# Performance work log

Hardware: AMD Instinct MI355X
Metric: run time of the kernel (lower is better)

## Reference

```python
import jax, jax.numpy as jnp
import numpy as np

INF = 99999.0  # sentinel used by the original torch module


def _dtw_table(x, y):
    """Full (N+1, M+1) DTW DP table, identical math to the torch double loop.

    Row recurrence: r[j+1] = c[j] + min(prev[j+1], prev[j], r[j]).
    Rewritten as the min-plus linear recurrence r[j+1] = min(a[j] + r[j], b[j])
    with a[j] = c[j], b[j] = c[j] + min(prev[j+1], prev[j]), which is
    associative and solved per-row with lax.associative_scan (wavefront-free
    parallelism within each row); rows advance with lax.scan.
    """
    M = y.shape[0]
    dt = x.dtype
    row0 = jnp.full((M + 1,), INF, dtype=dt).at[0].set(0.0)  # dtw[0, :]
    inf1 = jnp.full((1,), INF, dtype=dt)

    def combine(l, r):
        a1, b1 = l
        a2, b2 = r
        return (a1 + a2, jnp.minimum(a2 + b1, b2))

    def step(prev, xi):
        c = (xi - y) ** 2                              # (M,) squared cost
        m = jnp.minimum(prev[1:], prev[:-1])           # min(dtw[i,j+1], dtw[i,j])
        A, B = jax.lax.associative_scan(combine, (c, c + m))
        r = jnp.minimum(A + INF, B)                    # r[0] = INF folded in
        row = jnp.concatenate([inf1, r])               # dtw[i+1, :]
        return row, row

    _, rows = jax.lax.scan(step, row0, x)              # (N, M+1)
    table = jnp.concatenate([row0[None, :], rows], axis=0)
    return jnp.sqrt(table)


def setup_inputs() -> dict:
    key = jax.random.key(0)
    kx, ky = jax.random.split(key)
    N = M = 6144
    x = jax.random.normal(kx, (N,), dtype=jnp.float32)
    y = jax.random.normal(ky, (M,), dtype=jnp.float32)
    return {"x": x, "y": y}


def reference(x, y):
    return _dtw_table(x, y)
```

## Files before the change

### kernel.cpp

```cpp
#include <hip/hip_runtime.h>
#include <math.h>

#define NN    6144
#define MP1   6145
#define R     4
#define KC    4
#define WCH   (KC * 64)
#define GCH   (NN / WCH)
#define RTS   16
#define NWS   (NN / R)
#define STEPS (NWS + 63)
#define FINF  99999.0f

#define BR     384
#define NBI    (NN / BR)
#define TS2    (BR / R)
#define STEPS2 (TS2 + 63)

typedef float f4a __attribute__((ext_vector_type(4), aligned(4)));
typedef float f4v __attribute__((ext_vector_type(4), aligned(16)));

__device__ __forceinline__ float readlane_f(float v, int l) {
    return __int_as_float(__builtin_amdgcn_readlane(__float_as_int(v), l));
}
__device__ __forceinline__ float shup1(float v) {
    return __int_as_float(__builtin_amdgcn_update_dpp(
        0, __float_as_int(v), 0x138, 0xF, 0xF, false));
}

__global__ void __launch_bounds__(64) dtw_bnd(const float* __restrict__ x,
                                              const float* __restrict__ y,
                                              int* __restrict__ flags,
                                              float* __restrict__ bnd,
                                              float* __restrict__ rowb) {
    const int g    = blockIdx.x;
    const int lane = threadIdx.x;
    const int j0   = g * WCH;
    const int c0   = j0 + lane * KC;

    float yv[KC], cur[KC];
#pragma unroll
    for (int q = 0; q < KC; ++q) {
        yv[q]  = y[c0 + q];
        cur[q] = FINF;
    }
    float pl = (c0 == 0) ? 0.0f : FINF;
    float rlast[R];
#pragma unroll
    for (int r = 0; r < R; ++r) rlast[r] = FINF;
    float vbuf = FINF, vnext = FINF;

    const float4* x4 = (const float4*)x;
    float4 xw  = x4[lane];
    float4 xwN = x4[64 + lane];
    float xcur[R];
#pragma unroll
    for (int r = 0; r < R; ++r) xcur[r] = x[r];

    float cnx[R][KC];
#pragma unroll
    for (int r = 0; r < R; ++r)
#pragma unroll
        for (int q = 0; q < KC; ++q) {
            const float d = xcur[r] - yv[q];
            cnx[r][q] = d * d;
        }

    if (g != 0) {
        while (__hip_atomic_load(&flags[(g - 1) * 16], __ATOMIC_ACQUIRE,
                                 __HIP_MEMORY_SCOPE_AGENT) < 1) {
            __builtin_amdgcn_s_sleep(1);
        }
        vnext = bnd[(size_t)(g - 1) * NN + lane];
    }

    for (int s = 0; s < STEPS; ++s) {
        if (g != 0 && s < NWS && (s & (RTS - 1)) == 0) vbuf = vnext;

        if (g != 0 && (s & (RTS - 1)) == RTS - 4 && (s + 4) < NWS) {
            const int want = ((s + 4) >> 4) + 1;
            while (__hip_atomic_load(&flags[(g - 1) * 16], __ATOMIC_ACQUIRE,
                                     __HIP_MEMORY_SCOPE_AGENT) < want) {
                __builtin_amdgcn_s_sleep(1);
            }
            vnext = bnd[(size_t)(g - 1) * NN + (size_t)R * (s + 4) + lane];
        }

        float vin[R];
#pragma unroll
        for (int r = 0; r < R; ++r) {
            const float up = shup1(rlast[r]);
            const float vb = readlane_f(vbuf, ((s & (RTS - 1)) << 2) + r);
            const float l0 = (g == 0) ? FINF : vb;
            vin[r] = (lane == 0) ? l0 : up;
        }

        const bool active = (s >= lane) && (s - lane < NWS);
        if (active) {
#pragma unroll
            for (int r = 0; r < R; ++r) {
                float rl  = vin[r];
                float pm1 = (r == 0) ? pl : vin[r - 1];
                float nv[KC];
#pragma unroll
                for (int q = 0; q < KC; ++q) {
                    const float upv = cur[q];
                    rl     = cnx[r][q] + fminf(fminf(rl, upv), pm1);
                    pm1    = upv;
                    cur[q] = rl;
                    nv[q]  = rl;
                }
                rlast[r] = rl;
                if (r == R - 1) {
                    const int tp1 = s - lane + 1;
                    const int k   = tp1 / 96;
                    if (k * 96 == tp1 && k >= 1 && k <= NBI - 1) {
                        *(f4a*)&rowb[(size_t)k * MP1 + c0 + 1] =
                            (f4a){nv[0], nv[1], nv[2], nv[3]};
                    }
                }
            }
            pl = vin[R - 1];
            if (lane == 63) {
                *(f4a*)&bnd[(size_t)g * NN + R * (s - 63)] =
                    (f4a){rlast[0], rlast[1], rlast[2], rlast[3]};
            }
        }

        const int sn = s + 1;
        if ((sn & 63) == 0) {
            xw = xwN;
            int nb = sn + 64 + lane;
            if (nb > NN / 4 - 1) nb = NN / 4 - 1;
            xwN = x4[nb];
        }
        const float* xwp = (const float*)&xw;
#pragma unroll
        for (int r = 0; r < R; ++r) {
            const float xs = shup1(xcur[r]);
            const float xj = readlane_f(xwp[r], sn & 63);
            xcur[r] = (lane == 0) ? xj : xs;
        }
#pragma unroll
        for (int r = 0; r < R; ++r)
#pragma unroll
            for (int q = 0; q < KC; ++q) {
                const float d = xcur[r] - yv[q];
                cnx[r][q] = d * d;
            }

        if (g != GCH - 1 && s > 62 && ((s - 62) & (RTS - 1)) == 0) {
            if (lane == 0)
                __hip_atomic_store(&flags[g * 16], (s - 62) >> 4,
                                   __ATOMIC_RELEASE, __HIP_MEMORY_SCOPE_AGENT);
        }
    }
}

__global__ void __launch_bounds__(64) dtw_tile(const float* __restrict__ x,
                                               const float* __restrict__ y,
                                               const float* __restrict__ bnd,
                                               const float* __restrict__ rowb,
                                               float* __restrict__ out) {
    const int bj   = blockIdx.x;
    const int bi   = blockIdx.y;
    const int lane = threadIdx.x;

    __shared__ float left_s[BR];
    __shared__ float top_s[WCH + 1];
    __shared__ float xb_s[BR];

    for (int k = 0; k < BR / 64; ++k) {
        const int i = 64 * k + lane;
        left_s[i] = (bj == 0) ? FINF
                              : bnd[(size_t)(bj - 1) * NN + BR * bi + i];
        xb_s[i] = x[BR * bi + i];
    }
    for (int c = lane; c < WCH + 1; c += 64) {
        float tv;
        if (bi == 0)      tv = (bj == 0 && c == 0) ? 0.0f : FINF;
        else if (c == 0 && bj == 0) tv = FINF;
        else              tv = rowb[(size_t)bi * MP1 + WCH * bj + c];
        top_s[c] = tv;
    }
    __syncthreads();

    const int c0 = WCH * bj + KC * lane;
    float yv[KC], cur[KC];
#pragma unroll
    for (int q = 0; q < KC; ++q) {
        yv[q]  = y[c0 + q];
        cur[q] = top_s[KC * lane + q + 1];
    }
    float pl = top_s[KC * lane];
    float rlast[R];
#pragma unroll
    for (int r = 0; r < R; ++r) rlast[r] = FINF;

    float xcur[R];
#pragma unroll
    for (int r = 0; r < R; ++r) xcur[r] = xb_s[r];
    float cnx[R][KC];
#pragma unroll
    for (int r = 0; r < R; ++r)
#pragma unroll
        for (int q = 0; q < KC; ++q) {
            const float d = xcur[r] - yv[q];
            cnx[r][q] = d * d;
        }

    int off = (BR * bi + 1 - R * lane) * MP1 + c0 + 1;

    for (int s = 0; s < STEPS2; ++s) {
        float vin[R];
#pragma unroll
        for (int r = 0; r < R; ++r) {
            const float up = shup1(rlast[r]);
            const int  li  = R * s + r;
            const float l0 = left_s[li < BR ? li : BR - 1];
            vin[r] = (lane == 0) ? l0 : up;
        }

        const int  t      = s - lane;
        const bool active = (t >= 0) && (t < TS2);
        if (active) {
#pragma unroll
            for (int r = 0; r < R; ++r) {
                float rl  = vin[r];
                float pm1 = (r == 0) ? pl : vin[r - 1];
                float nv[KC];
#pragma unroll
                for (int q = 0; q < KC; ++q) {
                    const float upv = cur[q];
                    rl     = cnx[r][q] + fminf(fminf(rl, upv), pm1);
                    pm1    = upv;
                    cur[q] = rl;
                    nv[q]  = rl;
                }
                rlast[r] = rl;
                *(f4a*)(&out[off + r * MP1]) =
                    (f4a){__builtin_amdgcn_sqrtf(nv[0]),
                          __builtin_amdgcn_sqrtf(nv[1]),
                          __builtin_amdgcn_sqrtf(nv[2]),
                          __builtin_amdgcn_sqrtf(nv[3])};
            }
            pl = vin[R - 1];
        }
        off += R * MP1;

        const int sn = s + 1;
#pragma unroll
        for (int r = 0; r < R; ++r) {
            const float xs = shup1(xcur[r]);
            const int  xi  = R * sn + r;
            const float xj = xb_s[xi < BR ? xi : BR - 1];
            xcur[r] = (lane == 0) ? xj : xs;
        }
#pragma unroll
        for (int r = 0; r < R; ++r)
#pragma unroll
            for (int q = 0; q < KC; ++q) {
                const float d = xcur[r] - yv[q];
                cnx[r][q] = d * d;
            }
    }
}

__global__ void dtw_edges(float* __restrict__ out, float ev) {
    const int idx = blockIdx.x * blockDim.x + threadIdx.x;
    if (idx <= NN) {
        out[idx] = (idx == 0) ? 0.0f : ev;
        if (idx >= 1) out[(size_t)idx * MP1] = ev;
    }
}

extern "C" void kernel_launch(void* const* d_in, const int* in_sizes, int n_in,
                              void* d_out, int out_size, void* d_ws, size_t ws_size,
                              hipStream_t stream) {
    (void)in_sizes; (void)n_in; (void)out_size; (void)ws_size;
    const float* x = (const float*)d_in[0];
    const float* y = (const float*)d_in[1];
    float* out     = (float*)d_out;
    int* flags     = (int*)d_ws;

    const size_t bnd_off  = 4096;
    const size_t bnd_sz   = (size_t)GCH * NN * sizeof(float);
    const size_t rowb_off = bnd_off + bnd_sz;
    float* bnd  = (float*)((char*)d_ws + bnd_off);
    float* rowb = (float*)((char*)d_ws + rowb_off);

    hipMemsetAsync(flags, 0, GCH * 16 * sizeof(int), stream);

    dtw_edges<<<(MP1 + 255) / 256, 256, 0, stream>>>(out, sqrtf(FINF));
    dtw_bnd<<<GCH, 64, 0, stream>>>(x, y, flags, bnd, rowb);
    dtw_tile<<<dim3(GCH, NBI), 64, 0, stream>>>(x, y, bnd, rowb, out);
}
```

Measured before the change: 1.763 ms.

## Enlarge per-lane DTW tiles to 8x8 in boundary pass and 4x8 in tile pass

The boundary kernel now gives each lane an 8x8 cell block instead of 4x4. This halves the number of wavefront groups and the number of diagonal steps, so there are fewer cross-lane shuffles, less flag traffic and a shorter serial dependency chain. The flag publish moves to the start of the loop, and a final flag store is added after the loop. The tile kernel uses 8 columns per lane, giving 512-wide tiles, half as many blocks and longer per-lane chains. The trade-off is more registers per lane and longer serial chains within each step, which could cut latency hiding and parallelism in the tile kernel.

```diff
diff --git a/kernel.cpp b/kernel.cpp
--- a/kernel.cpp
+++ b/kernel.cpp
@@ -3,18 +3,22 @@
 
 #define NN    6144
 #define MP1   6145
-#define R     4
-#define KC    4
-#define WCH   (KC * 64)
-#define GCH   (NN / WCH)
-#define RTS   16
-#define NWS   (NN / R)
-#define STEPS (NWS + 63)
 #define FINF  99999.0f
 
+#define R1     8
+#define KC1    8
+#define WCH1   (KC1 * 64)
+#define GCH1   (NN / WCH1)
+#define RTS1   8
+#define NWS1   (NN / R1)
+#define STEPS1 (NWS1 + 63)
+
+#define R2     4
+#define KC2    8
+#define WCH2   (KC2 * 64)
 #define BR     384
 #define NBI    (NN / BR)
-#define TS2    (BR / R)
+#define TS2    (BR / R2)
 #define STEPS2 (TS2 + 63)
 
 typedef float f4a __attribute__((ext_vector_type(4), aligned(4)));
@@ -35,33 +39,34 @@
                                               float* __restrict__ rowb) {
     const int g    = blockIdx.x;
     const int lane = threadIdx.x;
-    const int j0   = g * WCH;
-    const int c0   = j0 + lane * KC;
-
-    float yv[KC], cur[KC];
-#pragma unroll
-    for (int q = 0; q < KC; ++q) {
+    const int c0   = g * WCH1 + lane * KC1;
+
+    float yv[KC1], cur[KC1];
+#pragma unroll
+    for (int q = 0; q < KC1; ++q) {
         yv[q]  = y[c0 + q];
         cur[q] = FINF;
     }
     float pl = (c0 == 0) ? 0.0f : FINF;
-    float rlast[R];
-#pragma unroll
-    for (int r = 0; r < R; ++r) rlast[r] = FINF;
+    float rlast[R1];
+#pragma unroll
+    for (int r = 0; r < R1; ++r) rlast[r] = FINF;
     float vbuf = FINF, vnext = FINF;
 
     const float4* x4 = (const float4*)x;
-    float4 xw  = x4[lane];
-    float4 xwN = x4[64 + lane];
-    float xcur[R];
-#pragma unroll
-    for (int r = 0; r < R; ++r) xcur[r] = x[r];
-
-    float cnx[R][KC];
-#pragma unroll
-    for (int r = 0; r < R; ++r)
-#pragma unroll
-        for (int q = 0; q < KC; ++q) {
+    float4 xwA  = x4[2 * lane];
+    float4 xwB  = x4[2 * lane + 1];
+    float4 xwAN = x4[2 * (64 + lane)];
+    float4 xwBN = x4[2 * (64 + lane) + 1];
+    float xcur[R1];
+#pragma unroll
+    for (int r = 0; r < R1; ++r) xcur[r] = x[r];
+
+    float cnx[R1][KC1];
+#pragma unroll
+    for (int r = 0; r < R1; ++r)
+#pragma unroll
+        for (int q = 0; q < KC1; ++q) {
             const float d = xcur[r] - yv[q];
             cnx[r][q] = d * d;
         }
@@ -74,36 +79,43 @@
         vnext = bnd[(size_t)(g - 1) * NN + lane];
     }
 
-    for (int s = 0; s < STEPS; ++s) {
-        if (g != 0 && s < NWS && (s & (RTS - 1)) == 0) vbuf = vnext;
-
-        if (g != 0 && (s & (RTS - 1)) == RTS - 4 && (s + 4) < NWS) {
-            const int want = ((s + 4) >> 4) + 1;
+    for (int s = 0; s < STEPS1; ++s) {
+        if (g != GCH1 - 1 && s > 64 && ((s - 64) & (RTS1 - 1)) == 0) {
+            if (lane == 0)
+                __hip_atomic_store(&flags[g * 16], (s - 64) >> 3,
+                                   __ATOMIC_RELEASE, __HIP_MEMORY_SCOPE_AGENT);
+        }
+
+        if (g != 0 && s < NWS1 && (s & (RTS1 - 1)) == 0) vbuf = vnext;
+
+        if (g != 0 && (s & (RTS1 - 1)) == RTS1 - 4 && (s + 4) < NWS1) {
+            const int want = ((s + 4) >> 3) + 1;
             while (__hip_atomic_load(&flags[(g - 1) * 16], __ATOMIC_ACQUIRE,
                                      __HIP_MEMORY_SCOPE_AGENT) < want) {
                 __builtin_amdgcn_s_sleep(1);
             }
-            vnext = bnd[(size_t)(g - 1) * NN + (size_t)R * (s + 4) + lane];
-        }
-
-        float vin[R];
-#pragma unroll
-        for (int r = 0; r < R; ++r) {
+            vnext = bnd[(size_t)(g - 1) * NN + (size_t)R1 * (s + 4) + lane];
+        }
+
+        float vin[R1];
+#pragma unroll
+        for (int r = 0; r < R1; ++r) {
             const float up = shup1(rlast[r]);
-            const float vb = readlane_f(vbuf, ((s & (RTS - 1)) << 2) + r);
+            const float vb = readlane_f(vbuf, ((s & (RTS1 - 1)) << 3) + r);
             const float l0 = (g == 0) ? FINF : vb;
             vin[r] = (lane == 0) ? l0 : up;
         }
 
-        const bool active = (s >= lane) && (s - lane < NWS);
+        const int  t      = s - lane;
+        const bool active = (t >= 0) && (t < NWS1);
         if (active) {
 #pragma unroll
-            for (int r = 0; r < R; ++r) {
+            for (int r = 0; r < R1; ++r) {
                 float rl  = vin[r];
                 float pm1 = (r == 0) ? pl : vin[r - 1];
-                float nv[KC];
-#pragma unroll
-                for (int q = 0; q < KC; ++q) {
+                float nv[KC1];
+#pragma unroll
+                for (int q = 0; q < KC1; ++q) {
                     const float upv = cur[q];
                     rl     = cnx[r][q] + fminf(fminf(rl, upv), pm1);
                     pm1    = upv;
@@ -111,49 +123,61 @@
                     nv[q]  = rl;
                 }
                 rlast[r] = rl;
-                if (r == R - 1) {
-                    const int tp1 = s - lane + 1;
-                    const int k   = tp1 / 96;
-                    if (k * 96 == tp1 && k >= 1 && k <= NBI - 1) {
+                if (r == R1 - 1) {
+                    const int tp1 = t + 1;
+                    const int k   = tp1 / 48;
+                    if (k * 48 == tp1 && k >= 1 && k <= NBI - 1) {
                         *(f4a*)&rowb[(size_t)k * MP1 + c0 + 1] =
                             (f4a){nv[0], nv[1], nv[2], nv[3]};
+                        *(f4a*)&rowb[(size_t)k * MP1 + c0 + 5] =
+                            (f4a){nv[4], nv[5], nv[6], nv[7]};
                     }
                 }
             }
-            pl = vin[R - 1];
+            pl = vin[R1 - 1];
             if (lane == 63) {
-                *(f4a*)&bnd[(size_t)g * NN + R * (s - 63)] =
-                    (f4a){rlast[0], rlast[1], rlast[2], rlast[3]};
+                *(f4v*)&bnd[(size_t)g * NN + (size_t)R1 * t] =
+                    (f4v){rlast[0], rlast[1], rlast[2], rlast[3]};
+                *(f4v*)&bnd[(size_t)g * NN + (size_t)R1 * t + 4] =
+                    (f4v){rlast[4], rlast[5], rlast[6], rlast[7]};
             }
         }
 
         const int sn = s + 1;
         if ((sn & 63) == 0) {
-            xw = xwN;
+            xwA = xwAN;
+            xwB = xwBN;
             int nb = sn + 64 + lane;
-            if (nb > NN / 4 - 1) nb = NN / 4 - 1;
-            xwN = x4[nb];
-        }
-        const float* xwp = (const float*)&xw;
-#pragma unroll
-        for (int r = 0; r < R; ++r) {
+            if (nb > NN / 8 - 1) nb = NN / 8 - 1;
+            xwAN = x4[2 * nb];
+            xwBN = x4[2 * nb + 1];
+        }
+        const float* xap = (const float*)&xwA;
+        const float* xbp = (const float*)&xwB;
+#pragma unroll
+        for (int r = 0; r < 4; ++r) {
             const float xs = shup1(xcur[r]);
-            const float xj = readlane_f(xwp[r], sn & 63);
+            const float xj = readlane_f(xap[r], sn & 63);
             xcur[r] = (lane == 0) ? xj : xs;
         }
 #pragma unroll
-        for (int r = 0; r < R; ++r)
-#pragma unroll
-            for (int q = 0; q < KC; ++q) {
+        for (int r = 4; r < 8; ++r) {
+            const float xs = shup1(xcur[r]);
+            const float xj = readlane_f(xbp[r - 4], sn & 63);
+            xcur[r] = (lane == 0) ? xj : xs;
+        }
+#pragma unroll
+        for (int r = 0; r < R1; ++r)
+#pragma unroll
+            for (int q = 0; q < KC1; ++q) {
                 const float d = xcur[r] - yv[q];
                 cnx[r][q] = d * d;
             }
-
-        if (g != GCH - 1 && s > 62 && ((s - 62) & (RTS - 1)) == 0) {
-            if (lane == 0)
-                __hip_atomic_store(&flags[g * 16], (s - 62) >> 4,
-                                   __ATOMIC_RELEASE, __HIP_MEMORY_SCOPE_AGENT);
-        }
+    }
+
+    if (g != GCH1 - 1 && lane == 0) {
+        __hip_atomic_store(&flags[g * 16], NWS1 >> 3,
+                           __ATOMIC_RELEASE, __HIP_MEMORY_SCOPE_AGENT);
     }
 }
 
@@ -167,56 +191,57 @@
     const int lane = threadIdx.x;
 
     __shared__ float left_s[BR];
-    __shared__ float top_s[WCH + 1];
+    __shared__ float top_s[WCH2 + 1];
     __shared__ float xb_s[BR];
 
+#pragma unroll
     for (int k = 0; k < BR / 64; ++k) {
         const int i = 64 * k + lane;
         left_s[i] = (bj == 0) ? FINF
                               : bnd[(size_t)(bj - 1) * NN + BR * bi + i];
         xb_s[i] = x[BR * bi + i];
     }
-    for (int c = lane; c < WCH + 1; c += 64) {
+    for (int c = lane; c < WCH2 + 1; c += 64) {
         float tv;
-        if (bi == 0)      tv = (bj == 0 && c == 0) ? 0.0f : FINF;
+        if (bi == 0)                tv = (bj == 0 && c == 0) ? 0.0f : FINF;
         else if (c == 0 && bj == 0) tv = FINF;
-        else              tv = rowb[(size_t)bi * MP1 + WCH * bj + c];
+        else                        tv = rowb[(size_t)bi * MP1 + WCH2 * bj + c];
         top_s[c] = tv;
     }
     __syncthreads();
 
-    const int c0 = WCH * bj + KC * lane;
-    float yv[KC], cur[KC];
-#pragma unroll
-    for (int q = 0; q < KC; ++q) {
+    const int c0 = WCH2 * bj + KC2 * lane;
+    float yv[KC2], cur[KC2];
+#pragma unroll
+    for (int q = 0; q < KC2; ++q) {
         yv[q]  = y[c0 + q];
-        cur[q] = top_s[KC * lane + q + 1];
-    }
-    float pl = top_s[KC * lane];
-    float rlast[R];
-#pragma unroll
-    for (int r = 0; r < R; ++r) rlast[r] = FINF;
-
-    float xcur[R];
-#pragma unroll
-    for (int r = 0; r < R; ++r) xcur[r] = xb_s[r];
-    float cnx[R][KC];
-#pragma unroll
-    for (int r = 0; r < R; ++r)
-#pragma unroll
-        for (int q = 0; q < KC; ++q) {
+        cur[q] = top_s[KC2 * lane + q + 1];
+    }
+    float pl = top_s[KC2 * lane];
+    float rlast[R2];
+#pragma unroll
+    for (int r = 0; r < R2; ++r) rlast[r] = FINF;
+
+    float xcur[R2];
+#pragma unroll
+    for (int r = 0; r < R2; ++r) xcur[r] = xb_s[r];
+    float cnx[R2][KC2];
+#pragma unroll
+    for (int r = 0; r < R2; ++r)
+#pragma unroll
+        for (int q = 0; q < KC2; ++q) {
             const float d = xcur[r] - yv[q];
             cnx[r][q] = d * d;
         }
 
-    int off = (BR * bi + 1 - R * lane) * MP1 + c0 + 1;
+    int off = (BR * bi + 1 - R2 * lane) * MP1 + c0 + 1;
 
     for (int s = 0; s < STEPS2; ++s) {
-        float vin[R];
-#pragma unroll
-        for (int r = 0; r < R; ++r) {
+        float vin[R2];
+#pragma unroll
+        for (int r = 0; r < R2; ++r) {
             const float up = shup1(rlast[r]);
-            const int  li  = R * s + r;
+            const int  li  = R2 * s + r;
             const float l0 = left_s[li < BR ? li : BR - 1];
             vin[r] = (lane == 0) ? l0 : up;
         }
@@ -225,12 +250,12 @@
         const bool active = (t >= 0) && (t < TS2);
         if (active) {
 #pragma unroll
-            for (int r = 0; r < R; ++r) {
+            for (int r = 0; r < R2; ++r) {
                 float rl  = vin[r];
                 float pm1 = (r == 0) ? pl : vin[r - 1];
-                float nv[KC];
-#pragma unroll
-                for (int q = 0; q < KC; ++q) {
+                float nv[KC2];
+#pragma unroll
+                for (int q = 0; q < KC2; ++q) {
                     const float upv = cur[q];
                     rl     = cnx[r][q] + fminf(fminf(rl, upv), pm1);
                     pm1    = upv;
@@ -243,23 +268,28 @@
                           __builtin_amdgcn_sqrtf(nv[1]),
                           __builtin_amdgcn_sqrtf(nv[2]),
                           __builtin_amdgcn_sqrtf(nv[3])};
-            }
-            pl = vin[R - 1];
-        }
-        off += R * MP1;
+                *(f4a*)(&out[off + r * MP1 + 4]) =
+                    (f4a){__builtin_amdgcn_sqrtf(nv[4]),
+                          __builtin_amdgcn_sqrtf(nv[5]),
+                          __builtin_amdgcn_sqrtf(nv[6]),
+                          __builtin_amdgcn_sqrtf(nv[7])};
+            }
+            pl = vin[R2 - 1];
+        }
+        off += R2 * MP1;
 
         const int sn = s + 1;
 #pragma unroll
-        for (int r = 0; r < R; ++r) {
+        for (int r = 0; r < R2; ++r) {
             const float xs = shup1(xcur[r]);
-            const int  xi  = R * sn + r;
+            const int  xi  = R2 * sn + r;
             const float xj = xb_s[xi < BR ? xi : BR - 1];
             xcur[r] = (lane == 0) ? xj : xs;
         }
 #pragma unroll
-        for (int r = 0; r < R; ++r)
-#pragma unroll
-            for (int q = 0; q < KC; ++q) {
+        for (int r = 0; r < R2; ++r)
+#pragma unroll
+            for (int q = 0; q < KC2; ++q) {
                 const float d = xcur[r] - yv[q];
                 cnx[r][q] = d * d;
             }
@@ -284,14 +314,14 @@
     int* flags     = (int*)d_ws;
 
     const size_t bnd_off  = 4096;
-    const size_t bnd_sz   = (size_t)GCH * NN * sizeof(float);
+    const size_t bnd_sz   = (size_t)GCH1 * NN * sizeof(float);
     const size_t rowb_off = bnd_off + bnd_sz;
     float* bnd  = (float*)((char*)d_ws + bnd_off);
     float* rowb = (float*)((char*)d_ws + rowb_off);
 
-    hipMemsetAsync(flags, 0, GCH * 16 * sizeof(int), stream);
+    hipMemsetAsync(flags, 0, GCH1 * 16 * sizeof(int), stream);
 
     dtw_edges<<<(MP1 + 255) / 256, 256, 0, stream>>>(out, sqrtf(FINF));
-    dtw_bnd<<<GCH, 64, 0, stream>>>(x, y, flags, bnd, rowb);
-    dtw_tile<<<dim3(GCH, NBI), 64, 0, stream>>>(x, y, bnd, rowb, out);
-}
+    dtw_bnd<<<GCH1, 64, 0, stream>>>(x, y, flags, bnd, rowb);
+    dtw_tile<<<dim3(GCH1, NBI), 64, 0, stream>>>(x, y, bnd, rowb, out);
+}
```

New measurement: 1.571 ms. 1.12x faster.
